# Kernel tuning notes

Hardware: AMD Instinct MI355X
Metric: run time of the kernel (lower is better)

Reference implementation:

```python
import jax, jax.numpy as jnp
import numpy as np

EMBED = 1024
N, L = 8, 1024


def setup_inputs() -> dict:
    key = jax.random.key(0)
    ks = jax.random.split(key, 6)
    return {
        "values": jax.random.normal(ks[0], (N, L, EMBED), dtype=jnp.float32),
        "keys": jax.random.normal(ks[1], (N, L, EMBED), dtype=jnp.float32),
        "query": jax.random.normal(ks[2], (N, L, EMBED), dtype=jnp.float32),
        "mask": jax.random.randint(ks[3], (N, 1, L, L), 0, 2, dtype=jnp.int32),
        "W_out": jax.random.normal(ks[4], (EMBED, EMBED), dtype=jnp.float32) * (EMBED ** -0.5),
        "b_out": jax.random.normal(ks[5], (EMBED,), dtype=jnp.float32) * 0.01,
        "heads": 16,
    }


def reference(values, keys, query, mask, W_out, b_out, heads):
    n, q_len, embed = query.shape
    k_len = keys.shape[1]
    v_len = values.shape[1]
    head_dim = embed // heads
    # split heads: (N, len, H, D)
    v = values.reshape(n, v_len, heads, head_dim)
    k = keys.reshape(n, k_len, heads, head_dim)
    q = query.reshape(n, q_len, heads, head_dim)
    # raw dot-product scores (note: the original module never applies its Q/K/V linears)
    energy = jnp.einsum('nqhd,nkhd->nhqk', q, k)  # (N, H, Q, K)
    # faithful quirk: masked positions set to +1e-20 (not -inf), BEFORE scaling
    energy = jnp.where(mask == 0, jnp.float32(1e-20), energy)
    # faithful quirk: scale by sqrt(embed_size), not sqrt(head_dim)
    attention = jax.nn.softmax(energy / jnp.sqrt(jnp.float32(embed)), axis=3)
    out = jnp.einsum('nhqk,nkhd->nqhd', attention, v).reshape(n, q_len, embed)
    # fc_out: torch Linear stores weight (out, in); y = x @ W^T + b
    return out @ W_out.T + b_out
```

## Files before the change

kernel.cpp:

```cpp
#include <hip/hip_runtime.h>
#include <hip/hip_bf16.h>

typedef __attribute__((ext_vector_type(8))) short bf16x8;
typedef __attribute__((ext_vector_type(4))) float f32x4;

#define SWZ(row, byteofs) (((row)*128) + ((byteofs) ^ (((row)&7)<<4)))

__device__ __forceinline__ unsigned pk2(float a, float b){
  __hip_bfloat162 h = __float22bfloat162_rn(make_float2(a, b));
  unsigned u; __builtin_memcpy(&u, &h, 4);
  return u;
}

__device__ __forceinline__ void gld16(const void* g, void* l){
  __builtin_amdgcn_global_load_lds((const __attribute__((address_space(1))) void*)g,
                                   (__attribute__((address_space(3))) void*)l, 16, 0, 0);
}

union bfpack { bf16x8 v; unsigned u[4]; uint4 q; };

__global__ __launch_bounds__(256) void mask_bits_kernel(const int* __restrict__ mask,
                                                        unsigned* __restrict__ bits){
  int t = blockIdx.x * 256 + threadIdx.x;
  int u = t >> 6;
  int lane = t & 63;
  int row = u >> 4;
  int chunk = u & 15;
  int m = mask[(size_t)row * 1024 + chunk * 64 + lane];
  unsigned long long b = __ballot(m != 0);
  if (lane == 0){
    unsigned* p = bits + row * 32 + chunk * 2;
    p[0] = (unsigned)(b & 0xffffffffull);
    p[1] = (unsigned)(b >> 32);
  }
}

__global__ __launch_bounds__(256) void wconv_kernel(const float* __restrict__ W,
                                                    unsigned short* __restrict__ Wb){
  int i = blockIdx.x * 256 + threadIdx.x;
  float4 f = reinterpret_cast<const float4*>(W)[i];
  uint2 o = make_uint2(pk2(f.x, f.y), pk2(f.z, f.w));
  reinterpret_cast<uint2*>(Wb)[i] = o;
}

__global__ __launch_bounds__(256) void permqk_kernel(const float* __restrict__ src,
                                                     unsigned short* __restrict__ dst){
  int w = blockIdx.x * 4 + (threadIdx.x >> 6);
  int lane = threadIdx.x & 63;
  int n = w >> 11, h = (w >> 7) & 15, l8 = w & 127;
  int l = l8 * 8 + (lane >> 3);
  int dch = (lane & 7) * 8;
  const float* sp = src + ((size_t)n * 1024 + l) * 1024 + h * 64 + dch;
  float4 a = *reinterpret_cast<const float4*>(sp);
  float4 b = *reinterpret_cast<const float4*>(sp + 4);
  uint4 o = make_uint4(pk2(a.x,a.y), pk2(a.z,a.w), pk2(b.x,b.y), pk2(b.z,b.w));
  *reinterpret_cast<uint4*>(dst + (((size_t)n * 16 + h) * 1024 + l) * 64 + dch) = o;
}

__global__ __launch_bounds__(256) void permv_kernel(const float* __restrict__ src,
                                                    unsigned short* __restrict__ dst){
  __shared__ __attribute__((aligned(16))) unsigned short T[64*64];
  int bid = blockIdx.x;
  int n = bid >> 8, h = (bid >> 4) & 15, l0 = (bid & 15) * 64;
  int t = threadIdx.x;
  {
    int l = t >> 2, dseg = t & 3;
    const float* sp = src + ((size_t)n * 1024 + l0 + l) * 1024 + h * 64 + dseg * 16;
    float4 f0 = *reinterpret_cast<const float4*>(sp + 0);
    float4 f1 = *reinterpret_cast<const float4*>(sp + 4);
    float4 f2 = *reinterpret_cast<const float4*>(sp + 8);
    float4 f3 = *reinterpret_cast<const float4*>(sp + 12);
    uint4 lo = make_uint4(pk2(f0.x,f0.y), pk2(f0.z,f0.w), pk2(f1.x,f1.y), pk2(f1.z,f1.w));
    uint4 hi = make_uint4(pk2(f2.x,f2.y), pk2(f2.z,f2.w), pk2(f3.x,f3.y), pk2(f3.z,f3.w));
    *reinterpret_cast<uint4*>((char*)T + SWZ(l, dseg*32))      = lo;
    *reinterpret_cast<uint4*>((char*)T + SWZ(l, dseg*32 + 16)) = hi;
  }
  __syncthreads();
  {
    int d = t >> 2, lseg = t & 3;
    for (int j = 0; j < 2; ++j){
      bf16x8 wv;
      #pragma unroll
      for (int i = 0; i < 8; ++i){
        int l = lseg*16 + j*8 + i;
        wv[i] = *(const short*)((const char*)T + (size_t)l*128 + ((d*2) ^ (i<<4)));
      }
      *reinterpret_cast<bf16x8*>(dst + (((size_t)n * 16 + h) * 64 + d) * 1024 + l0 + lseg*16 + j*8) = wv;
    }
  }
}

__global__ __launch_bounds__(256) void attn_kernel(
    const float* __restrict__ Q, const unsigned short* __restrict__ Kb,
    const unsigned short* __restrict__ Vtg, const unsigned* __restrict__ bits,
    unsigned short* __restrict__ Obf)
{
  __shared__ __attribute__((aligned(16))) unsigned short Kt[2][64*64];
  __shared__ __attribute__((aligned(16))) unsigned short Vt[2][64*64];
  __shared__ __attribute__((aligned(16))) unsigned short Pl[4][16*64];

  int bid = blockIdx.x;
  int wg = ((bid & 7) << 8) | (bid >> 3);
  int qb = wg & 15, h = (wg >> 4) & 15, n = wg >> 8;

  int tid = threadIdx.x, wid = tid >> 6, lane = tid & 63, lg = lane >> 4, lc = lane & 15;
  int qbase = qb * 64 + wid * 16;

  const unsigned short* Kh = Kb  + ((size_t)(n*16 + h)) * 1024 * 64;
  const unsigned short* Vh = Vtg + ((size_t)(n*16 + h)) * 64 * 1024;

  bf16x8 qf[2];
  {
    const float* qp = Q + (size_t)(n*1024 + qbase + lc) * 1024 + h*64;
    #pragma unroll
    for (int c = 0; c < 2; ++c){
      float4 a0 = *reinterpret_cast<const float4*>(qp + c*32 + lg*8);
      float4 a1 = *reinterpret_cast<const float4*>(qp + c*32 + lg*8 + 4);
      bfpack pk;
      pk.u[0] = pk2(a0.x,a0.y); pk.u[1] = pk2(a0.z,a0.w);
      pk.u[2] = pk2(a1.x,a1.y); pk.u[3] = pk2(a1.z,a1.w);
      qf[c] = pk.v;
    }
  }

  const int s0 = tid, s1 = tid + 256;
  const int r0 = s0 >> 3, c0 = ((s0 & 7) * 16) ^ ((r0 & 7) << 4);
  const int r1 = s1 >> 3, c1 = ((s1 & 7) * 16) ^ ((r1 & 7) << 4);

#define STAGE(KB, BUF) do { \
    gld16((const char*)Kh + ((size_t)((KB)*64 + r0) * 128 + c0), (char*)Kt[BUF] + s0*16); \
    gld16((const char*)Kh + ((size_t)((KB)*64 + r1) * 128 + c1), (char*)Kt[BUF] + s1*16); \
    gld16((const char*)Vh + ((size_t)r0 * 2048 + (KB)*128 + c0), (char*)Vt[BUF] + s0*16); \
    gld16((const char*)Vh + ((size_t)r1 * 2048 + (KB)*128 + c1), (char*)Vt[BUF] + s1*16); \
  } while(0)

  f32x4 acc[4];
  for (int i = 0; i < 4; ++i) acc[i] = (f32x4){0.f,0.f,0.f,0.f};
  float lsum[4] = {0.f,0.f,0.f,0.f};
  const float scale = 0.03125f;

  STAGE(0, 0);
  int cur = 0;

  for (int kb = 0; kb < 16; ++kb){
    __syncthreads();
    if (kb < 15) STAGE(kb + 1, cur ^ 1);

    unsigned words[4][2];
    {
      const unsigned* bp = bits + (size_t)(n*1024 + qbase + lg*4) * 32 + kb*2;
      #pragma unroll
      for (int r = 0; r < 4; ++r){ words[r][0] = bp[r*32]; words[r][1] = bp[r*32 + 1]; }
    }

    f32x4 S[4];
    #pragma unroll
    for (int t = 0; t < 4; ++t) S[t] = (f32x4){0.f,0.f,0.f,0.f};
    __builtin_amdgcn_s_setprio(1);
    #pragma unroll
    for (int t = 0; t < 4; ++t)
      #pragma unroll
      for (int c = 0; c < 2; ++c){
        bf16x8 kf = *reinterpret_cast<const bf16x8*>((const char*)Kt[cur] + SWZ(t*16 + lc, lg*16 + c*64));
        S[t] = __builtin_amdgcn_mfma_f32_16x16x32_bf16(qf[c], kf, S[t], 0, 0, 0);
      }
    __builtin_amdgcn_s_setprio(0);

    float p[4][4];
    #pragma unroll
    for (int t = 0; t < 4; ++t){
      int bitidx = ((t & 1) << 4) + lc;
      #pragma unroll
      for (int r = 0; r < 4; ++r){
        bool mk = (words[r][t>>1] >> bitidx) & 1u;
        p[t][r] = mk ? __expf(S[t][r] * scale) : 1.0f;
      }
    }
    #pragma unroll
    for (int r = 0; r < 4; ++r)
      lsum[r] += (p[0][r] + p[1][r]) + (p[2][r] + p[3][r]);

    unsigned short* pl = &Pl[wid][0];
    #pragma unroll
    for (int t = 0; t < 4; ++t){
      unsigned w01 = pk2(p[t][0], p[t][1]);
      unsigned w23 = pk2(p[t][2], p[t][3]);
      int colb = (t*16 + lc)*2;
      *(unsigned short*)((char*)pl + SWZ(lg*4 + 0, colb)) = (unsigned short)w01;
      *(unsigned short*)((char*)pl + SWZ(lg*4 + 1, colb)) = (unsigned short)(w01 >> 16);
      *(unsigned short*)((char*)pl + SWZ(lg*4 + 2, colb)) = (unsigned short)w23;
      *(unsigned short*)((char*)pl + SWZ(lg*4 + 3, colb)) = (unsigned short)(w23 >> 16);
    }

    __builtin_amdgcn_s_setprio(1);
    #pragma unroll
    for (int kc = 0; kc < 2; ++kc){
      bf16x8 af = *reinterpret_cast<const bf16x8*>((const char*)pl + SWZ(lc, lg*16 + kc*64));
      #pragma unroll
      for (int t2 = 0; t2 < 4; ++t2){
        bf16x8 vf = *reinterpret_cast<const bf16x8*>((const char*)Vt[cur] + SWZ(t2*16 + lc, lg*16 + kc*64));
        acc[t2] = __builtin_amdgcn_mfma_f32_16x16x32_bf16(af, vf, acc[t2], 0, 0, 0);
      }
    }
    __builtin_amdgcn_s_setprio(0);
    cur ^= 1;
  }
#undef STAGE

  #pragma unroll
  for (int r = 0; r < 4; ++r){
    float s = lsum[r];
    for (int d = 1; d < 16; d <<= 1) s += __shfl_xor(s, d, 64);
    float inv = 1.0f / s;
    size_t qg = (size_t)(n*1024 + qbase + lg*4 + r);
    unsigned short* op = Obf + (qg * 16 + h) * 64;
    unsigned w01 = pk2(acc[0][r]*inv, acc[1][r]*inv);
    unsigned w23 = pk2(acc[2][r]*inv, acc[3][r]*inv);
    op[0*16 + lc] = (unsigned short)w01;
    op[1*16 + lc] = (unsigned short)(w01 >> 16);
    op[2*16 + lc] = (unsigned short)w23;
    op[3*16 + lc] = (unsigned short)(w23 >> 16);
  }
}

__global__ __launch_bounds__(256) void out_gemm_kernel(
    const unsigned short* __restrict__ A, const unsigned short* __restrict__ B,
    const float* __restrict__ bias, float* __restrict__ out)
{
  __shared__ __attribute__((aligned(16))) unsigned short As[2][128*64];
  __shared__ __attribute__((aligned(16))) unsigned short Bs[2][128*64];

  int mb = blockIdx.x;
  int nb = blockIdx.y;
  int tid = threadIdx.x, wid = tid >> 6, lane = tid & 63, lg = lane >> 4, lc = lane & 15;
  int wr = wid >> 1, wc = wid & 1;

  int rr[4], cc[4];
  #pragma unroll
  for (int i = 0; i < 4; ++i){
    int s = tid + 256*i;
    rr[i] = s >> 3;
    cc[i] = ((s & 7) * 16) ^ ((rr[i] & 7) << 4);
  }

#define GSTAGE(KB, BUF) do { \
    _Pragma("unroll") \
    for (int i = 0; i < 4; ++i){ \
      int s = tid + 256*i; \
      gld16((const char*)A + ((size_t)(mb*128 + rr[i]) * 1024 + (KB)*64) * 2 + cc[i], (char*)As[BUF] + s*16); \
      gld16((const char*)B + ((size_t)(nb*128 + rr[i]) * 1024 + (KB)*64) * 2 + cc[i], (char*)Bs[BUF] + s*16); \
    } \
  } while(0)

  f32x4 acc[4][4];
  for (int m = 0; m < 4; ++m)
    for (int nn2 = 0; nn2 < 4; ++nn2) acc[m][nn2] = (f32x4){0.f,0.f,0.f,0.f};

  GSTAGE(0, 0);
  int cur = 0;

  for (int kb = 0; kb < 16; ++kb){
    __syncthreads();
    if (kb < 15) GSTAGE(kb + 1, cur ^ 1);
    #pragma unroll
    for (int kc = 0; kc < 2; ++kc){
      bf16x8 af[4], bfr[4];
      #pragma unroll
      for (int m = 0; m < 4; ++m)
        af[m] = *reinterpret_cast<const bf16x8*>((const char*)As[cur] + SWZ(wr*64 + m*16 + lc, kc*64 + lg*16));
      #pragma unroll
      for (int nn2 = 0; nn2 < 4; ++nn2)
        bfr[nn2] = *reinterpret_cast<const bf16x8*>((const char*)Bs[cur] + SWZ(wc*64 + nn2*16 + lc, kc*64 + lg*16));
      __builtin_amdgcn_s_setprio(1);
      #pragma unroll
      for (int m = 0; m < 4; ++m)
        #pragma unroll
        for (int nn2 = 0; nn2 < 4; ++nn2)
          acc[m][nn2] = __builtin_amdgcn_mfma_f32_16x16x32_bf16(af[m], bfr[nn2], acc[m][nn2], 0, 0, 0);
      __builtin_amdgcn_s_setprio(0);
    }
    cur ^= 1;
  }
#undef GSTAGE

  for (int nn2 = 0; nn2 < 4; ++nn2){
    int col = nb*128 + wc*64 + nn2*16 + lc;
    float bv = bias[col];
    for (int m = 0; m < 4; ++m){
      int rowb = mb*128 + wr*64 + m*16 + lg*4;
      for (int r = 0; r < 4; ++r)
        out[(size_t)(rowb + r) * 1024 + col] = acc[m][nn2][r] + bv;
    }
  }
}

extern "C" void kernel_launch(void* const* d_in, const int* in_sizes, int n_in,
                              void* d_out, int out_size, void* d_ws, size_t ws_size,
                              hipStream_t stream) {
  const float* V  = (const float*)d_in[0];
  const float* K  = (const float*)d_in[1];
  const float* Q  = (const float*)d_in[2];
  const int* mask = (const int*)d_in[3];
  const float* W  = (const float*)d_in[4];
  const float* b  = (const float*)d_in[5];
  float* out = (float*)d_out;

  char* ws = (char*)d_ws;
  unsigned* bits       = (unsigned*)ws;
  unsigned short* Wb   = (unsigned short*)(ws + (1u<<20));
  unsigned short* Obf  = (unsigned short*)(ws + (3u<<20));
  unsigned short* Vtg  = (unsigned short*)(ws + (19u<<20));
  unsigned short* Kb   = (unsigned short*)d_out;

  mask_bits_kernel<<<32768, 256, 0, stream>>>(mask, bits);
  wconv_kernel<<<1024, 256, 0, stream>>>(W, Wb);
  permqk_kernel<<<4096, 256, 0, stream>>>(K, Kb);
  permv_kernel<<<2048, 256, 0, stream>>>(V, Vtg);
  attn_kernel<<<2048, 256, 0, stream>>>(Q, Kb, Vtg, bits, Obf);
  dim3 g(64, 8);
  out_gemm_kernel<<<g, 256, 0, stream>>>(Obf, Wb, b, out);
}
```

Before: 135.1 us.

## Process two 16-row query subtiles per wave to reuse K/V tiles

Each attention block now covers 128 query rows instead of 64. Every wave holds two 16-row Q fragments and issues two MFMAs for each K and V fragment it reads from LDS. This halves the grid and the global K/V staging traffic per query, and raises the MFMA-to-LDS-read ratio. The cost is more registers for the doubled accumulators and S tiles, a larger P scratch buffer, and fewer blocks to spread across CUs.

```diff
diff --git a/kernel.cpp b/kernel.cpp
--- a/kernel.cpp
+++ b/kernel.cpp
@@ -97,21 +97,22 @@
 {
   __shared__ __attribute__((aligned(16))) unsigned short Kt[2][64*64];
   __shared__ __attribute__((aligned(16))) unsigned short Vt[2][64*64];
-  __shared__ __attribute__((aligned(16))) unsigned short Pl[4][16*64];
+  __shared__ __attribute__((aligned(16))) unsigned short Pl[4][32*64];
 
   int bid = blockIdx.x;
-  int wg = ((bid & 7) << 8) | (bid >> 3);
-  int qb = wg & 15, h = (wg >> 4) & 15, n = wg >> 8;
+  int wg = ((bid & 7) << 7) | (bid >> 3);
+  int qb = wg & 7, h = (wg >> 3) & 15, n = wg >> 7;
 
   int tid = threadIdx.x, wid = tid >> 6, lane = tid & 63, lg = lane >> 4, lc = lane & 15;
-  int qbase = qb * 64 + wid * 16;
+  int qbase = qb * 128 + wid * 16;
 
   const unsigned short* Kh = Kb  + ((size_t)(n*16 + h)) * 1024 * 64;
   const unsigned short* Vh = Vtg + ((size_t)(n*16 + h)) * 64 * 1024;
 
-  bf16x8 qf[2];
-  {
-    const float* qp = Q + (size_t)(n*1024 + qbase + lc) * 1024 + h*64;
+  bf16x8 qf[2][2];
+  #pragma unroll
+  for (int s = 0; s < 2; ++s){
+    const float* qp = Q + (size_t)(n*1024 + qbase + s*64 + lc) * 1024 + h*64;
     #pragma unroll
     for (int c = 0; c < 2; ++c){
       float4 a0 = *reinterpret_cast<const float4*>(qp + c*32 + lg*8);
@@ -119,7 +120,7 @@
       bfpack pk;
       pk.u[0] = pk2(a0.x,a0.y); pk.u[1] = pk2(a0.z,a0.w);
       pk.u[2] = pk2(a1.x,a1.y); pk.u[3] = pk2(a1.z,a1.w);
-      qf[c] = pk.v;
+      qf[s][c] = pk.v;
     }
   }
 
@@ -134,9 +135,11 @@
     gld16((const char*)Vh + ((size_t)r1 * 2048 + (KB)*128 + c1), (char*)Vt[BUF] + s1*16); \
   } while(0)
 
-  f32x4 acc[4];
-  for (int i = 0; i < 4; ++i) acc[i] = (f32x4){0.f,0.f,0.f,0.f};
-  float lsum[4] = {0.f,0.f,0.f,0.f};
+  f32x4 acc[2][4];
+  #pragma unroll
+  for (int s = 0; s < 2; ++s)
+    for (int i = 0; i < 4; ++i) acc[s][i] = (f32x4){0.f,0.f,0.f,0.f};
+  float lsum[2][4] = {{0.f,0.f,0.f,0.f},{0.f,0.f,0.f,0.f}};
   const float scale = 0.03125f;
 
   STAGE(0, 0);
@@ -146,60 +149,69 @@
     __syncthreads();
     if (kb < 15) STAGE(kb + 1, cur ^ 1);
 
-    unsigned words[4][2];
-    {
-      const unsigned* bp = bits + (size_t)(n*1024 + qbase + lg*4) * 32 + kb*2;
-      #pragma unroll
-      for (int r = 0; r < 4; ++r){ words[r][0] = bp[r*32]; words[r][1] = bp[r*32 + 1]; }
-    }
-
-    f32x4 S[4];
-    #pragma unroll
-    for (int t = 0; t < 4; ++t) S[t] = (f32x4){0.f,0.f,0.f,0.f};
+    unsigned words[2][4][2];
+    #pragma unroll
+    for (int s = 0; s < 2; ++s){
+      const unsigned* bp = bits + (size_t)(n*1024 + qbase + s*64 + lg*4) * 32 + kb*2;
+      #pragma unroll
+      for (int r = 0; r < 4; ++r){ words[s][r][0] = bp[r*32]; words[s][r][1] = bp[r*32 + 1]; }
+    }
+
+    f32x4 S[2][4];
+    #pragma unroll
+    for (int s = 0; s < 2; ++s)
+      #pragma unroll
+      for (int t = 0; t < 4; ++t) S[s][t] = (f32x4){0.f,0.f,0.f,0.f};
     __builtin_amdgcn_s_setprio(1);
     #pragma unroll
     for (int t = 0; t < 4; ++t)
       #pragma unroll
       for (int c = 0; c < 2; ++c){
         bf16x8 kf = *reinterpret_cast<const bf16x8*>((const char*)Kt[cur] + SWZ(t*16 + lc, lg*16 + c*64));
-        S[t] = __builtin_amdgcn_mfma_f32_16x16x32_bf16(qf[c], kf, S[t], 0, 0, 0);
+        S[0][t] = __builtin_amdgcn_mfma_f32_16x16x32_bf16(qf[0][c], kf, S[0][t], 0, 0, 0);
+        S[1][t] = __builtin_amdgcn_mfma_f32_16x16x32_bf16(qf[1][c], kf, S[1][t], 0, 0, 0);
       }
     __builtin_amdgcn_s_setprio(0);
 
-    float p[4][4];
-    #pragma unroll
-    for (int t = 0; t < 4; ++t){
-      int bitidx = ((t & 1) << 4) + lc;
-      #pragma unroll
-      for (int r = 0; r < 4; ++r){
-        bool mk = (words[r][t>>1] >> bitidx) & 1u;
-        p[t][r] = mk ? __expf(S[t][r] * scale) : 1.0f;
+    unsigned short* pl = &Pl[wid][0];
+    #pragma unroll
+    for (int s = 0; s < 2; ++s){
+      #pragma unroll
+      for (int t = 0; t < 4; ++t){
+        int bitidx = ((t & 1) << 4) + lc;
+        float p0, p1, p2, p3;
+        {
+          bool m0 = (words[s][0][t>>1] >> bitidx) & 1u;
+          bool m1 = (words[s][1][t>>1] >> bitidx) & 1u;
+          bool m2 = (words[s][2][t>>1] >> bitidx) & 1u;
+          bool m3 = (words[s][3][t>>1] >> bitidx) & 1u;
+          p0 = m0 ? __expf(S[s][t][0] * scale) : 1.0f;
+          p1 = m1 ? __expf(S[s][t][1] * scale) : 1.0f;
+          p2 = m2 ? __expf(S[s][t][2] * scale) : 1.0f;
+          p3 = m3 ? __expf(S[s][t][3] * scale) : 1.0f;
+        }
+        lsum[s][0] += p0; lsum[s][1] += p1; lsum[s][2] += p2; lsum[s][3] += p3;
+        unsigned w01 = pk2(p0, p1);
+        unsigned w23 = pk2(p2, p3);
+        int colb = (t*16 + lc)*2;
+        int rb = s*16 + lg*4;
+        *(unsigned short*)((char*)pl + SWZ(rb + 0, colb)) = (unsigned short)w01;
+        *(unsigned short*)((char*)pl + SWZ(rb + 1, colb)) = (unsigned short)(w01 >> 16);
+        *(unsigned short*)((char*)pl + SWZ(rb + 2, colb)) = (unsigned short)w23;
+        *(unsigned short*)((char*)pl + SWZ(rb + 3, colb)) = (unsigned short)(w23 >> 16);
       }
     }
-    #pragma unroll
-    for (int r = 0; r < 4; ++r)
-      lsum[r] += (p[0][r] + p[1][r]) + (p[2][r] + p[3][r]);
-
-    unsigned short* pl = &Pl[wid][0];
-    #pragma unroll
-    for (int t = 0; t < 4; ++t){
-      unsigned w01 = pk2(p[t][0], p[t][1]);
-      unsigned w23 = pk2(p[t][2], p[t][3]);
-      int colb = (t*16 + lc)*2;
-      *(unsigned short*)((char*)pl + SWZ(lg*4 + 0, colb)) = (unsigned short)w01;
-      *(unsigned short*)((char*)pl + SWZ(lg*4 + 1, colb)) = (unsigned short)(w01 >> 16);
-      *(unsigned short*)((char*)pl + SWZ(lg*4 + 2, colb)) = (unsigned short)w23;
-      *(unsigned short*)((char*)pl + SWZ(lg*4 + 3, colb)) = (unsigned short)(w23 >> 16);
-    }
 
     __builtin_amdgcn_s_setprio(1);
     #pragma unroll
     for (int kc = 0; kc < 2; ++kc){
-      bf16x8 af = *reinterpret_cast<const bf16x8*>((const char*)pl + SWZ(lc, lg*16 + kc*64));
+      bf16x8 af0 = *reinterpret_cast<const bf16x8*>((const char*)pl + SWZ(lc,      lg*16 + kc*64));
+      bf16x8 af1 = *reinterpret_cast<const bf16x8*>((const char*)pl + SWZ(16 + lc, lg*16 + kc*64));
       #pragma unroll
       for (int t2 = 0; t2 < 4; ++t2){
         bf16x8 vf = *reinterpret_cast<const bf16x8*>((const char*)Vt[cur] + SWZ(t2*16 + lc, lg*16 + kc*64));
-        acc[t2] = __builtin_amdgcn_mfma_f32_16x16x32_bf16(af, vf, acc[t2], 0, 0, 0);
+        acc[0][t2] = __builtin_amdgcn_mfma_f32_16x16x32_bf16(af0, vf, acc[0][t2], 0, 0, 0);
+        acc[1][t2] = __builtin_amdgcn_mfma_f32_16x16x32_bf16(af1, vf, acc[1][t2], 0, 0, 0);
       }
     }
     __builtin_amdgcn_s_setprio(0);
@@ -208,18 +220,21 @@
 #undef STAGE
 
   #pragma unroll
-  for (int r = 0; r < 4; ++r){
-    float s = lsum[r];
-    for (int d = 1; d < 16; d <<= 1) s += __shfl_xor(s, d, 64);
-    float inv = 1.0f / s;
-    size_t qg = (size_t)(n*1024 + qbase + lg*4 + r);
-    unsigned short* op = Obf + (qg * 16 + h) * 64;
-    unsigned w01 = pk2(acc[0][r]*inv, acc[1][r]*inv);
-    unsigned w23 = pk2(acc[2][r]*inv, acc[3][r]*inv);
-    op[0*16 + lc] = (unsigned short)w01;
-    op[1*16 + lc] = (unsigned short)(w01 >> 16);
-    op[2*16 + lc] = (unsigned short)w23;
-    op[3*16 + lc] = (unsigned short)(w23 >> 16);
+  for (int s = 0; s < 2; ++s){
+    #pragma unroll
+    for (int r = 0; r < 4; ++r){
+      float ssum = lsum[s][r];
+      for (int d = 1; d < 16; d <<= 1) ssum += __shfl_xor(ssum, d, 64);
+      float inv = 1.0f / ssum;
+      size_t qg = (size_t)(n*1024 + qbase + s*64 + lg*4 + r);
+      unsigned short* op = Obf + (qg * 16 + h) * 64;
+      unsigned w01 = pk2(acc[s][0][r]*inv, acc[s][1][r]*inv);
+      unsigned w23 = pk2(acc[s][2][r]*inv, acc[s][3][r]*inv);
+      op[0*16 + lc] = (unsigned short)w01;
+      op[1*16 + lc] = (unsigned short)(w01 >> 16);
+      op[2*16 + lc] = (unsigned short)w23;
+      op[3*16 + lc] = (unsigned short)(w23 >> 16);
+    }
   }
 }
 
@@ -316,7 +331,7 @@
   wconv_kernel<<<1024, 256, 0, stream>>>(W, Wb);
   permqk_kernel<<<4096, 256, 0, stream>>>(K, Kb);
   permv_kernel<<<2048, 256, 0, stream>>>(V, Vtg);
-  attn_kernel<<<2048, 256, 0, stream>>>(Q, Kb, Vtg, bits, Obf);
+  attn_kernel<<<1024, 256, 0, stream>>>(Q, Kb, Vtg, bits, Obf);
   dim3 g(64, 8);
   out_gemm_kernel<<<g, 256, 0, stream>>>(Obf, Wb, b, out);
 }
```

After: 146.5 us. 8.5% more time.

## Replace double-buffered K/V staging with single-buffered split K and V loads

Applied to the files above, without the earlier changes.

The attention kernel drops the two-slot K/V shared-memory ring and uses one buffer each for K and V. Inside each iteration, V for the current block is fetched while QK^T and softmax run, and K for the next block is fetched while P·V runs. A second barrier per iteration separates the two phases. This cuts the kernel's LDS footprint, which can allow more resident workgroups per CU. The cost is shorter windows to hide load latency and an extra __syncthreads in every iteration.

```diff
diff --git a/kernel.cpp b/kernel.cpp
--- a/kernel.cpp
+++ b/kernel.cpp
@@ -95,8 +95,8 @@
     const unsigned short* __restrict__ Vtg, const unsigned* __restrict__ bits,
     unsigned short* __restrict__ Obf)
 {
-  __shared__ __attribute__((aligned(16))) unsigned short Kt[2][64*64];
-  __shared__ __attribute__((aligned(16))) unsigned short Vt[2][64*64];
+  __shared__ __attribute__((aligned(16))) unsigned short Kt[64*64];
+  __shared__ __attribute__((aligned(16))) unsigned short Vt[64*64];
   __shared__ __attribute__((aligned(16))) unsigned short Pl[4][16*64];
 
   int bid = blockIdx.x;
@@ -127,11 +127,13 @@
   const int r0 = s0 >> 3, c0 = ((s0 & 7) * 16) ^ ((r0 & 7) << 4);
   const int r1 = s1 >> 3, c1 = ((s1 & 7) * 16) ^ ((r1 & 7) << 4);
 
-#define STAGE(KB, BUF) do { \
-    gld16((const char*)Kh + ((size_t)((KB)*64 + r0) * 128 + c0), (char*)Kt[BUF] + s0*16); \
-    gld16((const char*)Kh + ((size_t)((KB)*64 + r1) * 128 + c1), (char*)Kt[BUF] + s1*16); \
-    gld16((const char*)Vh + ((size_t)r0 * 2048 + (KB)*128 + c0), (char*)Vt[BUF] + s0*16); \
-    gld16((const char*)Vh + ((size_t)r1 * 2048 + (KB)*128 + c1), (char*)Vt[BUF] + s1*16); \
+#define STAGE_K(KB) do { \
+    gld16((const char*)Kh + ((size_t)((KB)*64 + r0) * 128 + c0), (char*)Kt + s0*16); \
+    gld16((const char*)Kh + ((size_t)((KB)*64 + r1) * 128 + c1), (char*)Kt + s1*16); \
+  } while(0)
+#define STAGE_V(KB) do { \
+    gld16((const char*)Vh + ((size_t)r0 * 2048 + (KB)*128 + c0), (char*)Vt + s0*16); \
+    gld16((const char*)Vh + ((size_t)r1 * 2048 + (KB)*128 + c1), (char*)Vt + s1*16); \
   } while(0)
 
   f32x4 acc[4];
@@ -139,12 +141,11 @@
   float lsum[4] = {0.f,0.f,0.f,0.f};
   const float scale = 0.03125f;
 
-  STAGE(0, 0);
-  int cur = 0;
+  STAGE_K(0);
 
   for (int kb = 0; kb < 16; ++kb){
     __syncthreads();
-    if (kb < 15) STAGE(kb + 1, cur ^ 1);
+    STAGE_V(kb);
 
     unsigned words[4][2];
     {
@@ -161,7 +162,7 @@
     for (int t = 0; t < 4; ++t)
       #pragma unroll
       for (int c = 0; c < 2; ++c){
-        bf16x8 kf = *reinterpret_cast<const bf16x8*>((const char*)Kt[cur] + SWZ(t*16 + lc, lg*16 + c*64));
+        bf16x8 kf = *reinterpret_cast<const bf16x8*>((const char*)Kt + SWZ(t*16 + lc, lg*16 + c*64));
         S[t] = __builtin_amdgcn_mfma_f32_16x16x32_bf16(qf[c], kf, S[t], 0, 0, 0);
       }
     __builtin_amdgcn_s_setprio(0);
@@ -192,20 +193,23 @@
       *(unsigned short*)((char*)pl + SWZ(lg*4 + 3, colb)) = (unsigned short)(w23 >> 16);
     }
 
+    __syncthreads();
+    if (kb < 15) STAGE_K(kb+1);
+
     __builtin_amdgcn_s_setprio(1);
     #pragma unroll
     for (int kc = 0; kc < 2; ++kc){
       bf16x8 af = *reinterpret_cast<const bf16x8*>((const char*)pl + SWZ(lc, lg*16 + kc*64));
       #pragma unroll
       for (int t2 = 0; t2 < 4; ++t2){
-        bf16x8 vf = *reinterpret_cast<const bf16x8*>((const char*)Vt[cur] + SWZ(t2*16 + lc, lg*16 + kc*64));
+        bf16x8 vf = *reinterpret_cast<const bf16x8*>((const char*)Vt + SWZ(t2*16 + lc, lg*16 + kc*64));
         acc[t2] = __builtin_amdgcn_mfma_f32_16x16x32_bf16(af, vf, acc[t2], 0, 0, 0);
       }
     }
     __builtin_amdgcn_s_setprio(0);
-    cur ^= 1;
-  }
-#undef STAGE
+  }
+#undef STAGE_K
+#undef STAGE_V
 
   #pragma unroll
   for (int r = 0; r < 4; ++r){
```

Result: slower. 137.8 us (+2.0%).

## Merge four preprocessing kernels into one block-dispatched prep kernel

Applied to the files above, without the earlier changes.

Combines mask bit-packing, weight bf16 conversion, K permute/convert and V transpose/convert into a single launch that picks its work by block index. This removes three kernel launches and the idle gaps between them, and lets the independent passes run on the GPU at the same time. The mask packing also changes from a wave-wide ballot to each thread reading 16 ints with vector loads and writing a 16-bit word, which cuts the grid from 32768 to 2048 blocks. The bit layout must still match what the attention kernel expects, and the V blocks now share a kernel that reserves shared memory even for blocks that do not use it.

```diff
diff --git a/kernel.cpp b/kernel.cpp
--- a/kernel.cpp
+++ b/kernel.cpp
@@ -19,73 +19,72 @@
 
 union bfpack { bf16x8 v; unsigned u[4]; uint4 q; };
 
-__global__ __launch_bounds__(256) void mask_bits_kernel(const int* __restrict__ mask,
-                                                        unsigned* __restrict__ bits){
-  int t = blockIdx.x * 256 + threadIdx.x;
-  int u = t >> 6;
-  int lane = t & 63;
-  int row = u >> 4;
-  int chunk = u & 15;
-  int m = mask[(size_t)row * 1024 + chunk * 64 + lane];
-  unsigned long long b = __ballot(m != 0);
-  if (lane == 0){
-    unsigned* p = bits + row * 32 + chunk * 2;
-    p[0] = (unsigned)(b & 0xffffffffull);
-    p[1] = (unsigned)(b >> 32);
-  }
-}
-
-__global__ __launch_bounds__(256) void wconv_kernel(const float* __restrict__ W,
-                                                    unsigned short* __restrict__ Wb){
-  int i = blockIdx.x * 256 + threadIdx.x;
-  float4 f = reinterpret_cast<const float4*>(W)[i];
-  uint2 o = make_uint2(pk2(f.x, f.y), pk2(f.z, f.w));
-  reinterpret_cast<uint2*>(Wb)[i] = o;
-}
-
-__global__ __launch_bounds__(256) void permqk_kernel(const float* __restrict__ src,
-                                                     unsigned short* __restrict__ dst){
-  int w = blockIdx.x * 4 + (threadIdx.x >> 6);
-  int lane = threadIdx.x & 63;
-  int n = w >> 11, h = (w >> 7) & 15, l8 = w & 127;
-  int l = l8 * 8 + (lane >> 3);
-  int dch = (lane & 7) * 8;
-  const float* sp = src + ((size_t)n * 1024 + l) * 1024 + h * 64 + dch;
-  float4 a = *reinterpret_cast<const float4*>(sp);
-  float4 b = *reinterpret_cast<const float4*>(sp + 4);
-  uint4 o = make_uint4(pk2(a.x,a.y), pk2(a.z,a.w), pk2(b.x,b.y), pk2(b.z,b.w));
-  *reinterpret_cast<uint4*>(dst + (((size_t)n * 16 + h) * 1024 + l) * 64 + dch) = o;
-}
-
-__global__ __launch_bounds__(256) void permv_kernel(const float* __restrict__ src,
-                                                    unsigned short* __restrict__ dst){
+__global__ __launch_bounds__(256) void prep_kernel(
+    const int* __restrict__ mask, unsigned short* __restrict__ bits16,
+    const float* __restrict__ W, unsigned short* __restrict__ Wb,
+    const float* __restrict__ Ksrc, unsigned short* __restrict__ Kb,
+    const float* __restrict__ Vsrc, unsigned short* __restrict__ Vtg)
+{
   __shared__ __attribute__((aligned(16))) unsigned short T[64*64];
-  int bid = blockIdx.x;
-  int n = bid >> 8, h = (bid >> 4) & 15, l0 = (bid & 15) * 64;
-  int t = threadIdx.x;
-  {
-    int l = t >> 2, dseg = t & 3;
-    const float* sp = src + ((size_t)n * 1024 + l0 + l) * 1024 + h * 64 + dseg * 16;
-    float4 f0 = *reinterpret_cast<const float4*>(sp + 0);
-    float4 f1 = *reinterpret_cast<const float4*>(sp + 4);
-    float4 f2 = *reinterpret_cast<const float4*>(sp + 8);
-    float4 f3 = *reinterpret_cast<const float4*>(sp + 12);
-    uint4 lo = make_uint4(pk2(f0.x,f0.y), pk2(f0.z,f0.w), pk2(f1.x,f1.y), pk2(f1.z,f1.w));
-    uint4 hi = make_uint4(pk2(f2.x,f2.y), pk2(f2.z,f2.w), pk2(f3.x,f3.y), pk2(f3.z,f3.w));
-    *reinterpret_cast<uint4*>((char*)T + SWZ(l, dseg*32))      = lo;
-    *reinterpret_cast<uint4*>((char*)T + SWZ(l, dseg*32 + 16)) = hi;
-  }
-  __syncthreads();
-  {
-    int d = t >> 2, lseg = t & 3;
-    for (int j = 0; j < 2; ++j){
-      bf16x8 wv;
-      #pragma unroll
-      for (int i = 0; i < 8; ++i){
-        int l = lseg*16 + j*8 + i;
-        wv[i] = *(const short*)((const char*)T + (size_t)l*128 + ((d*2) ^ (i<<4)));
+  int bid = blockIdx.x, tid = threadIdx.x;
+
+  if (bid < 2048){
+    size_t i = (size_t)bid * 256 + tid;
+    const int4* mp = reinterpret_cast<const int4*>(mask) + i * 4;
+    int4 a = mp[0], b = mp[1], c = mp[2], d = mp[3];
+    unsigned m = 0;
+    m |= (a.x!=0) ? 1u<<0 : 0;  m |= (a.y!=0) ? 1u<<1 : 0;
+    m |= (a.z!=0) ? 1u<<2 : 0;  m |= (a.w!=0) ? 1u<<3 : 0;
+    m |= (b.x!=0) ? 1u<<4 : 0;  m |= (b.y!=0) ? 1u<<5 : 0;
+    m |= (b.z!=0) ? 1u<<6 : 0;  m |= (b.w!=0) ? 1u<<7 : 0;
+    m |= (c.x!=0) ? 1u<<8 : 0;  m |= (c.y!=0) ? 1u<<9 : 0;
+    m |= (c.z!=0) ? 1u<<10 : 0; m |= (c.w!=0) ? 1u<<11 : 0;
+    m |= (d.x!=0) ? 1u<<12 : 0; m |= (d.y!=0) ? 1u<<13 : 0;
+    m |= (d.z!=0) ? 1u<<14 : 0; m |= (d.w!=0) ? 1u<<15 : 0;
+    bits16[i] = (unsigned short)m;
+  } else if (bid < 3072){
+    int i = (bid - 2048) * 256 + tid;
+    float4 f = reinterpret_cast<const float4*>(W)[i];
+    uint2 o = make_uint2(pk2(f.x, f.y), pk2(f.z, f.w));
+    reinterpret_cast<uint2*>(Wb)[i] = o;
+  } else if (bid < 7168){
+    int w = (bid - 3072) * 4 + (tid >> 6);
+    int lane = tid & 63;
+    int n = w >> 11, h = (w >> 7) & 15, l8 = w & 127;
+    int l = l8 * 8 + (lane >> 3);
+    int dch = (lane & 7) * 8;
+    const float* sp = Ksrc + ((size_t)n * 1024 + l) * 1024 + h * 64 + dch;
+    float4 a = *reinterpret_cast<const float4*>(sp);
+    float4 b = *reinterpret_cast<const float4*>(sp + 4);
+    uint4 o = make_uint4(pk2(a.x,a.y), pk2(a.z,a.w), pk2(b.x,b.y), pk2(b.z,b.w));
+    *reinterpret_cast<uint4*>(Kb + (((size_t)n * 16 + h) * 1024 + l) * 64 + dch) = o;
+  } else {
+    int vb = bid - 7168;
+    int n = vb >> 8, h = (vb >> 4) & 15, l0 = (vb & 15) * 64;
+    {
+      int l = tid >> 2, dseg = tid & 3;
+      const float* sp = Vsrc + ((size_t)n * 1024 + l0 + l) * 1024 + h * 64 + dseg * 16;
+      float4 f0 = *reinterpret_cast<const float4*>(sp + 0);
+      float4 f1 = *reinterpret_cast<const float4*>(sp + 4);
+      float4 f2 = *reinterpret_cast<const float4*>(sp + 8);
+      float4 f3 = *reinterpret_cast<const float4*>(sp + 12);
+      uint4 lo = make_uint4(pk2(f0.x,f0.y), pk2(f0.z,f0.w), pk2(f1.x,f1.y), pk2(f1.z,f1.w));
+      uint4 hi = make_uint4(pk2(f2.x,f2.y), pk2(f2.z,f2.w), pk2(f3.x,f3.y), pk2(f3.z,f3.w));
+      *reinterpret_cast<uint4*>((char*)T + SWZ(l, dseg*32))      = lo;
+      *reinterpret_cast<uint4*>((char*)T + SWZ(l, dseg*32 + 16)) = hi;
+    }
+    __syncthreads();
+    {
+      int d = tid >> 2, lseg = tid & 3;
+      for (int j = 0; j < 2; ++j){
+        bf16x8 wv;
+        #pragma unroll
+        for (int i = 0; i < 8; ++i){
+          int l = lseg*16 + j*8 + i;
+          wv[i] = *(const short*)((const char*)T + (size_t)l*128 + ((d*2) ^ (i<<4)));
+        }
+        *reinterpret_cast<bf16x8*>(Vtg + (((size_t)n * 16 + h) * 64 + d) * 1024 + l0 + lseg*16 + j*8) = wv;
       }
-      *reinterpret_cast<bf16x8*>(dst + (((size_t)n * 16 + h) * 64 + d) * 1024 + l0 + lseg*16 + j*8) = wv;
     }
   }
 }
@@ -312,10 +311,7 @@
   unsigned short* Vtg  = (unsigned short*)(ws + (19u<<20));
   unsigned short* Kb   = (unsigned short*)d_out;
 
-  mask_bits_kernel<<<32768, 256, 0, stream>>>(mask, bits);
-  wconv_kernel<<<1024, 256, 0, stream>>>(W, Wb);
-  permqk_kernel<<<4096, 256, 0, stream>>>(K, Kb);
-  permv_kernel<<<2048, 256, 0, stream>>>(V, Vtg);
+  prep_kernel<<<9216, 256, 0, stream>>>(mask, (unsigned short*)bits, W, Wb, K, Kb, V, Vtg);
   attn_kernel<<<2048, 256, 0, stream>>>(Q, Kb, Vtg, bits, Obf);
   dim3 g(64, 8);
   out_gemm_kernel<<<g, 256, 0, stream>>>(Obf, Wb, b, out);
```

Result: faster. 122.4 us (median of 3 runs) (-9.4%).
